# Kernel tuning notes

Measured on AMD Instinct MI355X. Metric: run time of the kernel, lower is better.

## Reference

```python
import jax, jax.numpy as jnp
import numpy as np

CP = 1.0   # polynomial kernel balance (Kerv2d cp)
DP = 2     # polynomial kernel degree (Kerv2d dp)
EPS = 1e-5 # BatchNorm eps


def kerv2d(x, w, stride, padding):
    # polynomial kervolution: (patch . w + cp) ** dp, computed as conv then pointwise
    y = jax.lax.conv_general_dilated(
        x, w,
        window_strides=(stride, stride),
        padding=[(padding, padding), (padding, padding)],
        dimension_numbers=('NCHW', 'OIHW', 'NCHW'))
    return (y + CP) ** DP


def bn(x, g, b, m, v):
    # inference-mode BatchNorm2d with running stats, folded to scale/shift
    inv = g / jnp.sqrt(v + EPS)
    return x * inv[None, :, None, None] + (b - m * inv)[None, :, None, None]


def setup_inputs() -> dict:
    key = jax.random.key(0)
    ks = jax.random.split(key, 4)
    C_in, C_mid = 1024, 256  # bottleneck: 1024 -> 256 -> 256 -> 1024
    d = {
        'x':  jax.random.normal(ks[0], (128, C_in, 14, 14), jnp.float32),
        'w1': jax.random.normal(ks[1], (C_mid, C_in, 1, 1), jnp.float32) * 0.03,
        'w2': jax.random.normal(ks[2], (C_mid, C_mid, 3, 3), jnp.float32) * 0.02,
        'w3': jax.random.normal(ks[3], (C_in, C_mid, 1, 1), jnp.float32) * 0.03,
    }
    for i, c in zip((1, 2, 3), (C_mid, C_mid, C_in)):
        d[f'g{i}'] = jnp.ones((c,), jnp.float32)
        d[f'b{i}'] = jnp.zeros((c,), jnp.float32)
        d[f'm{i}'] = jnp.zeros((c,), jnp.float32)
        d[f'v{i}'] = jnp.ones((c,), jnp.float32)
    return d


def reference(x, w1, w2, w3, g1, b1, m1, v1, g2, b2, m2, v2, g3, b3, m3, v3):
    identity = x
    h = bn(kerv2d(x, w1, 1, 0), g1, b1, m1, v1)   # 1x1 kerv + BN (num_layers>34 branch)
    h = bn(kerv2d(h, w2, 1, 1), g2, b2, m2, v2)   # 3x3 kerv + BN, stride=1
    h = bn(kerv2d(h, w3, 1, 0), g3, b3, m3, v3)   # 1x1 kerv (expansion=4) + BN
    return h + identity                           # residual add (identity_downsample=None)
```

## Files before the change

kernel.cpp:

```cpp
#include <hip/hip_runtime.h>

using f32x4 = __attribute__((ext_vector_type(4))) float;
using s16x8 = __attribute__((ext_vector_type(8))) short;
using s16x4 = __attribute__((ext_vector_type(4))) short;

#define P_PIX 196
#define NPIX_ALL (128 * 196)
#define NROW  208
#define KT    32

static __device__ __forceinline__ short f2bf(float f) {
  union { float f; unsigned u; } a; a.f = f;
  unsigned u = a.u;
  u += 0x7fffu + ((u >> 16) & 1u);
  return (short)(u >> 16);
}

static __device__ __forceinline__ f32x4 mfma16(s16x8 a, s16x8 b, f32x4 c) {
  return __builtin_amdgcn_mfma_f32_16x16x32_bf16(a, b, c, 0, 0, 0);
}

static __device__ __forceinline__ void gload16(const short* g, short* l) {
  __builtin_amdgcn_global_load_lds(
      (const __attribute__((address_space(1))) unsigned int*)(g),
      (__attribute__((address_space(3))) unsigned int*)(l), 16, 0, 0);
}

static __device__ __forceinline__ const s16x8* fragp(const short* buf, int row, int l4) {
  return (const s16x8*)(buf + row * KT + ((l4 ^ ((row >> 1) & 3)) << 3));
}

static __device__ __forceinline__ void stage(const short* __restrict__ src, int srcK,
                                             int k0, short* dst, int rows, int rmax,
                                             int tid) {
  for (int t = tid; t < rows * 4; t += 256) {
    int r = t >> 2, c = t & 3;
    int rr = r < rmax ? r : rmax;
    int cs = c ^ ((r >> 1) & 3);
    gload16(src + (size_t)rr * srcK + k0 + cs * 8, dst + t * 8);
  }
}


__global__ void k_cvt4(const float* __restrict__ src, short* __restrict__ dst, int n4) {
  int i = blockIdx.x * 256 + threadIdx.x;
  if (i < n4) {
    f32x4 v = *(const f32x4*)(src + i * 4);
    s16x4 o;
    o[0] = f2bf(v[0]); o[1] = f2bf(v[1]); o[2] = f2bf(v[2]); o[3] = f2bf(v[3]);
    *(s16x4*)(dst + i * 4) = o;
  }
}

__global__ void k_w2t(const float* __restrict__ w2, short* __restrict__ W2t) {
  int i = blockIdx.x * 256 + threadIdx.x;
  if (i < 9 * 256 * 256) {
    int s = i >> 16, rem = i & 65535;
    int co = rem >> 8, ci = rem & 255;
    W2t[i] = f2bf(w2[(co * 256 + ci) * 9 + s]);
  }
}

__global__ void k_bn(const float* g1, const float* b1, const float* m1, const float* v1,
                     const float* g2, const float* b2, const float* m2, const float* v2,
                     const float* g3, const float* b3, const float* m3, const float* v3,
                     float* bn) {
  int t = blockIdx.x * 256 + threadIdx.x;
  if (t < 256) {
    float inv = g1[t] * rsqrtf(v1[t] + 1e-5f);
    bn[t] = inv; bn[256 + t] = b1[t] - m1[t] * inv;
  } else if (t < 512) {
    int c = t - 256;
    float inv = g2[c] * rsqrtf(v2[c] + 1e-5f);
    bn[512 + c] = inv; bn[768 + c] = b2[c] - m2[c] * inv;
  } else if (t < 1536) {
    int c = t - 512;
    float inv = g3[c] * rsqrtf(v3[c] + 1e-5f);
    bn[1024 + c] = inv; bn[2048 + c] = b3[c] - m3[c] * inv;
  }
}


__global__ __launch_bounds__(256) void k_layer1(
    const float* __restrict__ x, const short* __restrict__ W1b,
    const float* __restrict__ bnbuf, short* __restrict__ H1) {
  __shared__ __align__(16) short lB[2][128 * KT];
  const int tid = threadIdx.x;
  const int b = blockIdx.x;
  const int n = b >> 2, mb = (b >> 1) & 1, jh = b & 1;
  const int lane = tid & 63, wave = tid >> 6;
  const int l15 = lane & 15, l4 = lane >> 4;

  if (jh == 1 && tid < 96) {
    int bb = tid / 48, idx = tid % 48;
    s16x8 z = {0,0,0,0,0,0,0,0};
    *(s16x8*)(&lB[bb][100 * KT + idx * 8]) = z;
  }

  const float* xs = x + (size_t)n * 1024 * P_PIX;
  const short* Asrc = W1b + (size_t)(mb * 128) * 1024;

  const int npg = jh ? 25 : 28;
  const int pgbase = jh ? 24 : 0;
  const bool act = tid < npg * 8;
  const int pg = pgbase + (act ? tid % npg : 0);
  const int kg = act ? tid / npg : 0;
  const int lrow0 = pg * 4 - jh * 96;

  f32x4 rX[4], rY[4];
  auto loadx = [&](int kt, f32x4* r) {
    if (!act) return;
    const float* sp = xs + (size_t)(kt * 32 + kg * 4) * P_PIX + pg * 4;
    r[0] = *(const f32x4*)sp;
    r[1] = *(const f32x4*)(sp + P_PIX);
    r[2] = *(const f32x4*)(sp + 2 * P_PIX);
    r[3] = *(const f32x4*)(sp + 3 * P_PIX);
  };
  auto cvtw = [&](const f32x4* r, short* buf) {
    if (!act) return;
    int chunk = kg >> 1, inner = (kg & 1) * 4;
    #pragma unroll
    for (int q = 0; q < 4; ++q) {
      int lr = lrow0 + q;
      s16x4 w;
      w[0] = f2bf(r[0][q]); w[1] = f2bf(r[1][q]);
      w[2] = f2bf(r[2][q]); w[3] = f2bf(r[3][q]);
      *(s16x4*)(buf + lr * KT + ((chunk ^ ((lr >> 1) & 3)) << 3) + inner) = w;
    }
  };

  f32x4 acc[2][7];
  f32x4 zero = {0.f, 0.f, 0.f, 0.f};
  #pragma unroll
  for (int m = 0; m < 2; ++m)
    #pragma unroll
    for (int jj = 0; jj < 7; ++jj) acc[m][jj] = zero;

  loadx(0, rX);
  loadx(1, rY);
  cvtw(rX, lB[0]);
  __syncthreads();

  auto body = [&](int kt, f32x4* rNext, f32x4* rFill) {
    if (kt + 2 < 32) loadx(kt + 2, rFill);
    s16x8 a0 = *(const s16x8*)(Asrc + (size_t)(wave * 32 + l15) * 1024 + kt * 32 + l4 * 8);
    s16x8 a1 = *(const s16x8*)(Asrc + (size_t)(wave * 32 + 16 + l15) * 1024 + kt * 32 + l4 * 8);
    const short* B = lB[kt & 1];
    #pragma unroll
    for (int jj = 0; jj < 7; ++jj) {
      s16x8 bfr = *fragp(B, jj * 16 + l15, l4);
      acc[0][jj] = mfma16(a0, bfr, acc[0][jj]);
      acc[1][jj] = mfma16(a1, bfr, acc[1][jj]);
    }
    if (kt + 1 < 32) cvtw(rNext, lB[(kt + 1) & 1]);
    __syncthreads();
  };

  for (int kt = 0; kt < 32; kt += 2) {
    body(kt, rY, rX);
    body(kt + 1, rX, rY);
  }

  short* Hn = H1 + (size_t)n * P_PIX * 256;
  #pragma unroll
  for (int m = 0; m < 2; ++m) {
    int co = mb * 128 + wave * 32 + m * 16 + l4 * 4;
    f32x4 sc = *(const f32x4*)(bnbuf + co);
    f32x4 sh = *(const f32x4*)(bnbuf + 256 + co);
    #pragma unroll
    for (int jj = 0; jj < 7; ++jj) {
      if (jh && jj == 0) continue;
      int p = (jh * 6 + jj) * 16 + l15;
      if (p < P_PIX) {
        s16x4 o;
        #pragma unroll
        for (int i = 0; i < 4; ++i) {
          float y = acc[m][jj][i] + 1.0f;
          o[i] = f2bf(y * y * sc[i] + sh[i]);
        }
        *(s16x4*)(Hn + p * 256 + co) = o;
      }
    }
  }
}


__global__ __launch_bounds__(256) void k_layer2(
    const short* __restrict__ H1, const short* __restrict__ W2t,
    const float* __restrict__ bnbuf, short* __restrict__ H2) {
  __shared__ __align__(16) short lB[2][NROW * KT];
  const int tid = threadIdx.x;
  const int b = blockIdx.x;
  const int n = b >> 2, mb = (b >> 1) & 1, jh = b & 1;
  const int lane = tid & 63, wave = tid >> 6;
  const int l15 = lane & 15, l4 = lane >> 4;

  if (tid < 8) {
    int bb = tid >> 2, idx = tid & 3;
    s16x8 z = {0,0,0,0,0,0,0,0};
    *(s16x8*)(&lB[bb][196 * KT + idx * 8]) = z;
  }

  int vm[7];
  #pragma unroll
  for (int jj = 0; jj < 7; ++jj) {
    int p = (jh * 6 + jj) * 16 + l15;
    int m = 0;
    if (p < P_PIX) {
      int h = p / 14, w = p % 14;
      m = 2 | 16;
      if (h >= 1)  m |= 1;
      if (h < 13)  m |= 4;
      if (w >= 1)  m |= 8;
      if (w < 13)  m |= 32;
    }
    vm[jj] = m;
  }

  f32x4 acc[2][7];
  f32x4 zero = {0.f, 0.f, 0.f, 0.f};
  #pragma unroll
  for (int m = 0; m < 2; ++m)
    #pragma unroll
    for (int jj = 0; jj < 7; ++jj) acc[m][jj] = zero;

  const short* Bsrc = H1 + (size_t)n * P_PIX * 256;

  stage(Bsrc, 256, 0, lB[0], P_PIX, P_PIX - 1, tid);
  __syncthreads();

  for (int kt = 0; kt < 8; ++kt) {
    if (kt < 7)
      stage(Bsrc, 256, (kt + 1) * 32, lB[(kt + 1) & 1], P_PIX, P_PIX - 1, tid);
    const short* B = lB[kt & 1];
    #pragma unroll
    for (int s = 0; s < 9; ++s) {
      const int dy = s / 3, dx = s % 3;
      const int doff = (dy - 1) * 14 + (dx - 1);
      const size_t arow = (size_t)(s * 256 + mb * 128 + wave * 32 + l15) * 256 + kt * 32 + l4 * 8;
      s16x8 a0 = *(const s16x8*)(W2t + arow);
      s16x8 a1 = *(const s16x8*)(W2t + arow + 16 * 256);
      #pragma unroll
      for (int jj = 0; jj < 7; ++jj) {
        int p = (jh * 6 + jj) * 16 + l15;
        bool valid = ((vm[jj] >> dy) & 1) && ((vm[jj] >> (3 + dx)) & 1);
        int row = valid ? (p + doff) : 196;
        s16x8 bfr = *fragp(B, row, l4);
        acc[0][jj] = mfma16(a0, bfr, acc[0][jj]);
        acc[1][jj] = mfma16(a1, bfr, acc[1][jj]);
      }
    }
    __syncthreads();
  }

  short* Hn = H2 + (size_t)n * P_PIX * 256;
  #pragma unroll
  for (int m = 0; m < 2; ++m) {
    int co = mb * 128 + wave * 32 + m * 16 + l4 * 4;
    f32x4 sc = *(const f32x4*)(bnbuf + 512 + co);
    f32x4 sh = *(const f32x4*)(bnbuf + 768 + co);
    #pragma unroll
    for (int jj = 0; jj < 7; ++jj) {
      if (jh && jj == 0) continue;
      int p = (jh * 6 + jj) * 16 + l15;
      if (p < P_PIX) {
        s16x4 o;
        #pragma unroll
        for (int i = 0; i < 4; ++i) {
          float y = acc[m][jj][i] + 1.0f;
          o[i] = f2bf(y * y * sc[i] + sh[i]);
        }
        *(s16x4*)(Hn + p * 256 + co) = o;
      }
    }
  }
}


__global__ __launch_bounds__(256) void k_layer3(
    const short* __restrict__ H2, const short* __restrict__ W3b,
    const float* __restrict__ bnbuf, const float* __restrict__ x,
    float* __restrict__ out) {
  __shared__ __align__(16) short lB[2][NROW * KT];
  const int tid = threadIdx.x;
  const int tile = blockIdx.x >> 4, mb = blockIdx.x & 15;
  const int lane = tid & 63, wave = tid >> 6;
  const int l15 = lane & 15, l4 = lane >> 4;
  const int P0 = tile * NROW;
  const int rmax = NPIX_ALL - 1 - P0;

  const short* Asrc = W3b + (size_t)(mb * 64) * 256;
  const short* Bsrc = H2 + (size_t)P0 * 256;

  f32x4 acc[13];
  f32x4 zero = {0.f, 0.f, 0.f, 0.f};
  #pragma unroll
  for (int j = 0; j < 13; ++j) acc[j] = zero;

  stage(Bsrc, 256, 0, lB[0], NROW, rmax, tid);
  __syncthreads();

  for (int kt = 0; kt < 8; ++kt) {
    if (kt < 7)
      stage(Bsrc, 256, (kt + 1) * 32, lB[(kt + 1) & 1], NROW, rmax, tid);
    s16x8 a = *(const s16x8*)(Asrc + (size_t)(wave * 16 + l15) * 256 + kt * 32 + l4 * 8);
    const short* B = lB[kt & 1];
    #pragma unroll
    for (int j = 0; j < 13; ++j) {
      s16x8 bfr = *fragp(B, j * 16 + l15, l4);
      acc[j] = mfma16(a, bfr, acc[j]);
    }
    __syncthreads();
  }

  const int co = mb * 64 + wave * 16 + l4 * 4;
  f32x4 sc = *(const f32x4*)(bnbuf + 1024 + co);
  f32x4 sh = *(const f32x4*)(bnbuf + 2048 + co);

  #pragma unroll
  for (int bb = 0; bb < 3; ++bb) {
    const int jb = (bb == 0) ? 0 : (bb == 1 ? 5 : 9);
    const int jn = (bb == 0) ? 5 : 4;
    float xv[5][4];
    size_t bidx[5];
    bool okv[5];
    #pragma unroll
    for (int jj = 0; jj < 5; ++jj) {
      if (jj >= jn) break;
      int j = jb + jj;
      int P = P0 + j * 16 + l15;
      bool ok = P < NPIX_ALL;
      int nn = P / P_PIX, pp = P - nn * P_PIX;
      size_t bidxj = ((size_t)(nn * 1024 + co)) * P_PIX + pp;
      bidx[jj] = bidxj; okv[jj] = ok;
      #pragma unroll
      for (int i = 0; i < 4; ++i)
        xv[jj][i] = ok ? x[bidxj + (size_t)i * P_PIX] : 0.f;
    }
    #pragma unroll
    for (int jj = 0; jj < 5; ++jj) {
      if (jj >= jn) break;
      int j = jb + jj;
      if (okv[jj]) {
        #pragma unroll
        for (int i = 0; i < 4; ++i) {
          float y = acc[j][i] + 1.0f;
          out[bidx[jj] + (size_t)i * P_PIX] = y * y * sc[i] + sh[i] + xv[jj][i];
        }
      }
    }
  }
}


extern "C" void kernel_launch(void* const* d_in, const int* in_sizes, int n_in,
                              void* d_out, int out_size, void* d_ws, size_t ws_size,
                              hipStream_t stream) {
  (void)in_sizes; (void)n_in; (void)out_size; (void)ws_size;
  const float* x  = (const float*)d_in[0];
  const float* w1 = (const float*)d_in[1];
  const float* w2 = (const float*)d_in[2];
  const float* w3 = (const float*)d_in[3];
  const float* g1 = (const float*)d_in[4];
  const float* b1 = (const float*)d_in[5];
  const float* m1 = (const float*)d_in[6];
  const float* v1 = (const float*)d_in[7];
  const float* g2 = (const float*)d_in[8];
  const float* b2 = (const float*)d_in[9];
  const float* m2 = (const float*)d_in[10];
  const float* v2 = (const float*)d_in[11];
  const float* g3 = (const float*)d_in[12];
  const float* b3 = (const float*)d_in[13];
  const float* m3 = (const float*)d_in[14];
  const float* v3 = (const float*)d_in[15];

  char* ws = (char*)d_ws;
  short* W1b   = (short*)(ws + 0);
  short* W2t   = (short*)(ws + 524288);
  short* W3b   = (short*)(ws + 1703936);
  float* bnbuf = (float*)(ws + 2228224);
  short* H1    = (short*)(ws + 2240512);
  short* H2    = (short*)(ws + 15085568);

  k_cvt4<<<256, 256, 0, stream>>>(w1, W1b, 256 * 1024 / 4);
  k_cvt4<<<256, 256, 0, stream>>>(w3, W3b, 1024 * 256 / 4);
  k_w2t<<<2304, 256, 0, stream>>>(w2, W2t);
  k_bn<<<6, 256, 0, stream>>>(g1, b1, m1, v1, g2, b2, m2, v2, g3, b3, m3, v3, bnbuf);

  k_layer1<<<512, 256, 0, stream>>>(x, W1b, bnbuf, H1);
  k_layer2<<<512, 256, 0, stream>>>(H1, W2t, bnbuf, H2);
  k_layer3<<<1936, 256, 0, stream>>>(H2, W3b, bnbuf, x, (float*)d_out);
}
```

Baseline: 169.1 us.

## Merge prep kernels, pre-transpose x to bf16, and stage layer3 epilogue through LDS

The four weight/BN preparation kernels become one launch. When the workspace is large enough, x is first transposed to pixel-major bf16 so layer 1 can stage B tiles with async global-to-LDS loads. Otherwise the old layer 1 path is kept. The layer3 epilogue now writes accumulators to LDS so the residual reads and output writes become coalesced float4 accesses. The cost is an extra pass over x and one more kernel launch when the big path is taken.

```diff
diff --git a/kernel.cpp b/kernel.cpp
--- a/kernel.cpp
+++ b/kernel.cpp
@@ -42,41 +42,129 @@
 }
 
 
-__global__ void k_cvt4(const float* __restrict__ src, short* __restrict__ dst, int n4) {
+__global__ void k_prep(const float* __restrict__ w1, const float* __restrict__ w2,
+                       const float* __restrict__ w3,
+                       const float* g1, const float* b1, const float* m1, const float* v1,
+                       const float* g2, const float* b2, const float* m2, const float* v2,
+                       const float* g3, const float* b3, const float* m3, const float* v3,
+                       float* bn, short* W1b, short* W2t, short* W3b) {
   int i = blockIdx.x * 256 + threadIdx.x;
-  if (i < n4) {
-    f32x4 v = *(const f32x4*)(src + i * 4);
+  if (i < 65536) {
+    f32x4 v = *(const f32x4*)(w1 + i * 4);
     s16x4 o;
     o[0] = f2bf(v[0]); o[1] = f2bf(v[1]); o[2] = f2bf(v[2]); o[3] = f2bf(v[3]);
-    *(s16x4*)(dst + i * 4) = o;
-  }
-}
-
-__global__ void k_w2t(const float* __restrict__ w2, short* __restrict__ W2t) {
-  int i = blockIdx.x * 256 + threadIdx.x;
-  if (i < 9 * 256 * 256) {
-    int s = i >> 16, rem = i & 65535;
-    int co = rem >> 8, ci = rem & 255;
-    W2t[i] = f2bf(w2[(co * 256 + ci) * 9 + s]);
-  }
-}
-
-__global__ void k_bn(const float* g1, const float* b1, const float* m1, const float* v1,
-                     const float* g2, const float* b2, const float* m2, const float* v2,
-                     const float* g3, const float* b3, const float* m3, const float* v3,
-                     float* bn) {
-  int t = blockIdx.x * 256 + threadIdx.x;
-  if (t < 256) {
-    float inv = g1[t] * rsqrtf(v1[t] + 1e-5f);
-    bn[t] = inv; bn[256 + t] = b1[t] - m1[t] * inv;
-  } else if (t < 512) {
-    int c = t - 256;
-    float inv = g2[c] * rsqrtf(v2[c] + 1e-5f);
-    bn[512 + c] = inv; bn[768 + c] = b2[c] - m2[c] * inv;
-  } else if (t < 1536) {
-    int c = t - 512;
-    float inv = g3[c] * rsqrtf(v3[c] + 1e-5f);
-    bn[1024 + c] = inv; bn[2048 + c] = b3[c] - m3[c] * inv;
+    *(s16x4*)(W1b + i * 4) = o;
+  } else if (i < 131072) {
+    int q = i - 65536;
+    f32x4 v = *(const f32x4*)(w3 + q * 4);
+    s16x4 o;
+    o[0] = f2bf(v[0]); o[1] = f2bf(v[1]); o[2] = f2bf(v[2]); o[3] = f2bf(v[3]);
+    *(s16x4*)(W3b + q * 4) = o;
+  } else if (i < 278528) {
+    int q = (i - 131072) * 4;
+    s16x4 o;
+    #pragma unroll
+    for (int k = 0; k < 4; ++k) {
+      int idx = q + k;
+      int s = idx >> 16, rem = idx & 65535;
+      int co = rem >> 8, ci = rem & 255;
+      o[k] = f2bf(w2[(co * 256 + ci) * 9 + s]);
+    }
+    *(s16x4*)(W2t + q) = o;
+  } else if (i < 280064) {
+    int t = i - 278528;
+    if (t < 256) {
+      float inv = g1[t] * rsqrtf(v1[t] + 1e-5f);
+      bn[t] = inv; bn[256 + t] = b1[t] - m1[t] * inv;
+    } else if (t < 512) {
+      int c = t - 256;
+      float inv = g2[c] * rsqrtf(v2[c] + 1e-5f);
+      bn[512 + c] = inv; bn[768 + c] = b2[c] - m2[c] * inv;
+    } else {
+      int c = t - 512;
+      float inv = g3[c] * rsqrtf(v3[c] + 1e-5f);
+      bn[1024 + c] = inv; bn[2048 + c] = b3[c] - m3[c] * inv;
+    }
+  }
+}
+
+
+__global__ __launch_bounds__(256) void k_xpose(const float* __restrict__ x,
+                                               short* __restrict__ xb) {
+  const int n = blockIdx.x >> 4, cig = blockIdx.x & 15;
+  const int l = threadIdx.x & 63, w = threadIdx.x >> 6;
+  const float* xs = x + ((size_t)n * 1024 + cig * 64 + l) * P_PIX;
+  short* xd = xb + (size_t)n * P_PIX * 1024 + cig * 64 + l;
+  const int ni = (w == 0) ? 13 : 12;
+  for (int i = 0; i < ni; ++i) {
+    int pc = w + i * 4;
+    f32x4 v = *(const f32x4*)(xs + pc * 4);
+    #pragma unroll
+    for (int q = 0; q < 4; ++q)
+      xd[(size_t)(pc * 4 + q) * 1024] = f2bf(v[q]);
+  }
+}
+
+
+__global__ __launch_bounds__(256) void k_layer1b(
+    const short* __restrict__ xb, const short* __restrict__ W1b,
+    const float* __restrict__ bnbuf, short* __restrict__ H1) {
+  __shared__ __align__(16) short lB[2][112 * KT];
+  const int tid = threadIdx.x;
+  const int b = blockIdx.x;
+  const int n = b >> 2, mb = (b >> 1) & 1, jh = b & 1;
+  const int lane = tid & 63, wave = tid >> 6;
+  const int l15 = lane & 15, l4 = lane >> 4;
+
+  const short* Bsrc = xb + (size_t)(n * P_PIX + jh * 96) * 1024;
+  const short* Asrc = W1b + (size_t)(mb * 128) * 1024;
+  const int rmax = jh ? 99 : 111;
+
+  f32x4 acc[2][7];
+  f32x4 zero = {0.f, 0.f, 0.f, 0.f};
+  #pragma unroll
+  for (int m = 0; m < 2; ++m)
+    #pragma unroll
+    for (int jj = 0; jj < 7; ++jj) acc[m][jj] = zero;
+
+  stage(Bsrc, 1024, 0, lB[0], 112, rmax, tid);
+  __syncthreads();
+
+  for (int kt = 0; kt < 32; ++kt) {
+    if (kt < 31)
+      stage(Bsrc, 1024, (kt + 1) * 32, lB[(kt + 1) & 1], 112, rmax, tid);
+    s16x8 a0 = *(const s16x8*)(Asrc + (size_t)(wave * 32 + l15) * 1024 + kt * 32 + l4 * 8);
+    s16x8 a1 = *(const s16x8*)(Asrc + (size_t)(wave * 32 + 16 + l15) * 1024 + kt * 32 + l4 * 8);
+    const short* B = lB[kt & 1];
+    #pragma unroll
+    for (int jj = 0; jj < 7; ++jj) {
+      s16x8 bfr = *fragp(B, jj * 16 + l15, l4);
+      acc[0][jj] = mfma16(a0, bfr, acc[0][jj]);
+      acc[1][jj] = mfma16(a1, bfr, acc[1][jj]);
+    }
+    __syncthreads();
+  }
+
+  short* Hn = H1 + (size_t)n * P_PIX * 256;
+  #pragma unroll
+  for (int m = 0; m < 2; ++m) {
+    int co = mb * 128 + wave * 32 + m * 16 + l4 * 4;
+    f32x4 sc = *(const f32x4*)(bnbuf + co);
+    f32x4 sh = *(const f32x4*)(bnbuf + 256 + co);
+    #pragma unroll
+    for (int jj = 0; jj < 7; ++jj) {
+      if (jh && jj == 0) continue;
+      int p = (jh * 6 + jj) * 16 + l15;
+      if (p < P_PIX) {
+        s16x4 o;
+        #pragma unroll
+        for (int i = 0; i < 4; ++i) {
+          float y = acc[m][jj][i] + 1.0f;
+          o[i] = f2bf(y * y * sc[i] + sh[i]);
+        }
+        *(s16x4*)(Hn + p * 256 + co) = o;
+      }
+    }
   }
 }
 
@@ -281,7 +369,11 @@
     const short* __restrict__ H2, const short* __restrict__ W3b,
     const float* __restrict__ bnbuf, const float* __restrict__ x,
     float* __restrict__ out) {
-  __shared__ __align__(16) short lB[2][NROW * KT];
+  __shared__ __align__(16) char smem[27136];
+  short* const lB0 = (short*)smem;
+  short* const lB1 = lB0 + NROW * KT;
+  float* const eb = (float*)smem;
+
   const int tid = threadIdx.x;
   const int tile = blockIdx.x >> 4, mb = blockIdx.x & 15;
   const int lane = tid & 63, wave = tid >> 6;
@@ -297,14 +389,14 @@
   #pragma unroll
   for (int j = 0; j < 13; ++j) acc[j] = zero;
 
-  stage(Bsrc, 256, 0, lB[0], NROW, rmax, tid);
+  stage(Bsrc, 256, 0, lB0, NROW, rmax, tid);
   __syncthreads();
 
   for (int kt = 0; kt < 8; ++kt) {
     if (kt < 7)
-      stage(Bsrc, 256, (kt + 1) * 32, lB[(kt + 1) & 1], NROW, rmax, tid);
+      stage(Bsrc, 256, (kt + 1) * 32, ((kt + 1) & 1) ? lB1 : lB0, NROW, rmax, tid);
     s16x8 a = *(const s16x8*)(Asrc + (size_t)(wave * 16 + l15) * 256 + kt * 32 + l4 * 8);
-    const short* B = lB[kt & 1];
+    const short* B = (kt & 1) ? lB1 : lB0;
     #pragma unroll
     for (int j = 0; j < 13; ++j) {
       s16x8 bfr = *fragp(B, j * 16 + l15, l4);
@@ -313,39 +405,42 @@
     __syncthreads();
   }
 
-  const int co = mb * 64 + wave * 16 + l4 * 4;
-  f32x4 sc = *(const f32x4*)(bnbuf + 1024 + co);
-  f32x4 sh = *(const f32x4*)(bnbuf + 2048 + co);
-
-  #pragma unroll
-  for (int bb = 0; bb < 3; ++bb) {
-    const int jb = (bb == 0) ? 0 : (bb == 1 ? 5 : 9);
-    const int jn = (bb == 0) ? 5 : 4;
-    float xv[5][4];
-    size_t bidx[5];
-    bool okv[5];
-    #pragma unroll
-    for (int jj = 0; jj < 5; ++jj) {
-      if (jj >= jn) break;
-      int j = jb + jj;
-      int P = P0 + j * 16 + l15;
-      bool ok = P < NPIX_ALL;
-      int nn = P / P_PIX, pp = P - nn * P_PIX;
-      size_t bidxj = ((size_t)(nn * 1024 + co)) * P_PIX + pp;
-      bidx[jj] = bidxj; okv[jj] = ok;
+  const int co_r = tid >> 3;
+  const int pcb  = tid & 7;
+  #pragma unroll
+  for (int h = 0; h < 2; ++h) {
+    __syncthreads();
+    if ((wave >> 1) == h) {
+      const int co_l = (wave & 1) * 16 + l4 * 4;
       #pragma unroll
-      for (int i = 0; i < 4; ++i)
-        xv[jj][i] = ok ? x[bidxj + (size_t)i * P_PIX] : 0.f;
-    }
-    #pragma unroll
-    for (int jj = 0; jj < 5; ++jj) {
-      if (jj >= jn) break;
-      int j = jb + jj;
-      if (okv[jj]) {
+      for (int j = 0; j < 13; ++j) {
+        const int p = j * 16 + l15;
         #pragma unroll
-        for (int i = 0; i < 4; ++i) {
-          float y = acc[j][i] + 1.0f;
-          out[bidx[jj] + (size_t)i * P_PIX] = y * y * sc[i] + sh[i] + xv[jj][i];
+        for (int i = 0; i < 4; ++i)
+          eb[(co_l + i) * 212 + p] = acc[j][i];
+      }
+    }
+    __syncthreads();
+    const int co_g = mb * 64 + h * 32 + co_r;
+    const float scv = bnbuf[1024 + co_g];
+    const float shv = bnbuf[2048 + co_g];
+    #pragma unroll
+    for (int pass = 0; pass < 7; ++pass) {
+      const int pc = pcb + pass * 8;
+      if (pc < 52) {
+        const int P = P0 + pc * 4;
+        if (P < NPIX_ALL) {
+          f32x4 v = *(const f32x4*)(eb + co_r * 212 + pc * 4);
+          const int nn = P / P_PIX, pp = P - nn * P_PIX;
+          const size_t idx = ((size_t)(nn * 1024 + co_g)) * P_PIX + pp;
+          f32x4 xv = *(const f32x4*)(x + idx);
+          f32x4 o;
+          #pragma unroll
+          for (int k = 0; k < 4; ++k) {
+            float y = v[k] + 1.0f;
+            o[k] = y * y * scv + shv + xv[k];
+          }
+          *(f32x4*)(out + idx) = o;
         }
       }
     }
@@ -356,7 +451,7 @@
 extern "C" void kernel_launch(void* const* d_in, const int* in_sizes, int n_in,
                               void* d_out, int out_size, void* d_ws, size_t ws_size,
                               hipStream_t stream) {
-  (void)in_sizes; (void)n_in; (void)out_size; (void)ws_size;
+  (void)in_sizes; (void)n_in; (void)out_size;
   const float* x  = (const float*)d_in[0];
   const float* w1 = (const float*)d_in[1];
   const float* w2 = (const float*)d_in[2];
@@ -381,13 +476,18 @@
   float* bnbuf = (float*)(ws + 2228224);
   short* H1    = (short*)(ws + 2240512);
   short* H2    = (short*)(ws + 15085568);
-
-  k_cvt4<<<256, 256, 0, stream>>>(w1, W1b, 256 * 1024 / 4);
-  k_cvt4<<<256, 256, 0, stream>>>(w3, W3b, 1024 * 256 / 4);
-  k_w2t<<<2304, 256, 0, stream>>>(w2, W2t);
-  k_bn<<<6, 256, 0, stream>>>(g1, b1, m1, v1, g2, b2, m2, v2, g3, b3, m3, v3, bnbuf);
-
-  k_layer1<<<512, 256, 0, stream>>>(x, W1b, bnbuf, H1);
+  short* xb    = (short*)(ws + 15085568);
+  const bool big = ws_size >= 66465792ULL;
+
+  k_prep<<<1094, 256, 0, stream>>>(w1, w2, w3,
+                                   g1, b1, m1, v1, g2, b2, m2, v2, g3, b3, m3, v3,
+                                   bnbuf, W1b, W2t, W3b);
+  if (big) {
+    k_xpose<<<2048, 256, 0, stream>>>(x, xb);
+    k_layer1b<<<512, 256, 0, stream>>>(xb, W1b, bnbuf, H1);
+  } else {
+    k_layer1<<<512, 256, 0, stream>>>(x, W1b, bnbuf, H1);
+  }
   k_layer2<<<512, 256, 0, stream>>>(H1, W2t, bnbuf, H2);
   k_layer3<<<1936, 256, 0, stream>>>(H2, W3b, bnbuf, x, (float*)d_out);
 }
```

Result: slower. 180.9 us (+6.9%).
